# Kernel tuning notes

Measured on AMD Instinct MI355X. Metric: run time of the kernel, lower is better.

## Reference

```python
import jax, jax.numpy as jnp
import numpy as np

B, S, D = 2, 2048, 1024
H = 16
HD = D // H  # 64

def setup_inputs() -> dict:
    key = jax.random.key(0)
    ks = jax.random.split(key, 6)
    scale = 0.02
    x   = jax.random.normal(ks[0], (B, S, D), dtype=jnp.float32)
    Wq  = jax.random.normal(ks[1], (D, D), dtype=jnp.float32) * scale
    Wk  = jax.random.normal(ks[2], (D, D), dtype=jnp.float32) * scale
    Wv  = jax.random.normal(ks[3], (D, D), dtype=jnp.float32) * scale
    Wo  = jax.random.normal(ks[4], (D, D), dtype=jnp.float32) * scale
    bo  = jax.random.normal(ks[5], (D,), dtype=jnp.float32) * scale
    return {"x": x, "Wq": Wq, "Wk": Wk, "Wv": Wv, "Wo": Wo, "bo": bo}

def reference(x, Wq, Wk, Wv, Wo, bo):
    b, s, d = x.shape
    # QKV projections (no bias, qkv_bias=False); weights stored as [d_in, d_out]
    q = (x @ Wq).reshape(b, s, H, HD).transpose(0, 2, 1, 3)  # [b,h,s,hd]
    k = (x @ Wk).reshape(b, s, H, HD).transpose(0, 2, 1, 3)
    v = (x @ Wv).reshape(b, s, H, HD).transpose(0, 2, 1, 3)
    scores = jnp.einsum('bhqd,bhkd->bhqk', q, k)  # [b,h,s,s]
    causal = jnp.triu(jnp.ones((s, s), dtype=bool), k=1)
    scores = jnp.where(causal, -jnp.inf, scores)
    attn = jax.nn.softmax(scores / jnp.sqrt(jnp.float32(HD)), axis=-1)
    # dropout_rate = 0.0 -> identity
    ctx = jnp.einsum('bhqk,bhkd->bqhd', attn, v).reshape(b, s, d)
    return ctx @ Wo + bo
```

## Files before the change

kernel.cpp:

```cpp
#include <hip/hip_runtime.h>
#include <hip/hip_bf16.h>
#include <math.h>

#define B_ 2
#define S_ 2048
#define D_ 1024
#define H_ 16
#define HD_ 64
#define M_ (B_*S_)

typedef __attribute__((ext_vector_type(8))) short bf16x8;
typedef __attribute__((ext_vector_type(4))) float f32x4;

#define MFMA16(a,b,c) __builtin_amdgcn_mfma_f32_16x16x32_bf16(a,b,c,0,0,0)
#define INFF __builtin_inff()
#define LOG2E 1.44269504088896340736f
#define EXP2F(x) __builtin_amdgcn_exp2f(x)

static __device__ __forceinline__ unsigned short f2bf_bits(float f) {
    unsigned int u = __float_as_uint(f);
    unsigned int r = (u + 0x7fffu + ((u >> 16) & 1u)) >> 16;
    return (unsigned short)r;
}

static __device__ __forceinline__ unsigned cvt_pk_bf16(float a, float b) {
    unsigned r;
    asm("v_cvt_pk_bf16_f32 %0, %1, %2" : "=v"(r) : "v"(a), "v"(b));
    return r;
}

static __device__ __forceinline__ void gload16(const unsigned short* g, unsigned short* l) {
    __builtin_amdgcn_global_load_lds(
        (const __attribute__((address_space(1))) unsigned int*)(g),
        (__attribute__((address_space(3))) unsigned int*)(l),
        16, 0, 0);
}

#define BARR do { \
    __builtin_amdgcn_sched_barrier(0); \
    __builtin_amdgcn_s_barrier(); \
    __builtin_amdgcn_sched_barrier(0); \
} while (0)
#define LGK0 do { \
    asm volatile("s_waitcnt lgkmcnt(0)" ::: "memory"); \
    __builtin_amdgcn_sched_barrier(0); \
} while (0)
#define LGK8 do { \
    asm volatile("s_waitcnt lgkmcnt(8)" ::: "memory"); \
    __builtin_amdgcn_sched_barrier(0); \
} while (0)
#define VM6 do { \
    asm volatile("s_waitcnt vmcnt(6)" ::: "memory"); \
    __builtin_amdgcn_sched_barrier(0); \
} while (0)

__global__ __launch_bounds__(256) void convert_x_kernel(
    const float* __restrict__ x, unsigned short* __restrict__ o) {
    size_t i = (size_t)blockIdx.x * 256 + threadIdx.x;
    float4 v = reinterpret_cast<const float4*>(x)[i];
    ushort4 u;
    u.x = f2bf_bits(v.x); u.y = f2bf_bits(v.y);
    u.z = f2bf_bits(v.z); u.w = f2bf_bits(v.w);
    reinterpret_cast<ushort4*>(o)[i] = u;
}

__global__ __launch_bounds__(256) void convw_kernel(
    const float* __restrict__ W0, const float* __restrict__ W1,
    const float* __restrict__ W2, const float* __restrict__ W3,
    unsigned short* __restrict__ OT) {
    __shared__ float t[32][33];
    const float* W = (blockIdx.z == 0) ? W0 : (blockIdx.z == 1) ? W1
                    : (blockIdx.z == 2) ? W2 : W3;
    unsigned short* O = OT + (size_t)blockIdx.z * D_ * D_;
    int tx = threadIdx.x & 31, ty = threadIdx.x >> 5;
    int kb = blockIdx.y * 32, nb = blockIdx.x * 32;
#pragma unroll
    for (int i = 0; i < 4; i++)
        t[ty + 8*i][tx] = W[(size_t)(kb + ty + 8*i) * D_ + nb + tx];
    __syncthreads();
#pragma unroll
    for (int i = 0; i < 4; i++) {
        int n = nb + ty + 8*i, k = kb + tx;
        O[(size_t)n * D_ + k] = f2bf_bits(t[tx][ty + 8*i]);
    }
}

__global__ __launch_bounds__(512, 2) void gemm_qkv256(
    const unsigned short* __restrict__ A,
    const unsigned short* __restrict__ BT,
    unsigned short* __restrict__ outp)
{
    __shared__ union {
        struct { unsigned short A[2][2][8192]; unsigned short B[2][2][8192]; } s;
        unsigned short vt[256][136];
    } sm;
    const int tid = threadIdx.x, lane = tid & 63, wid = tid >> 6;
    const int lrow = lane & 15, lk8 = lane >> 4, orow = lk8 * 4;
    const int wmo = (wid >> 2) * 64;
    const int wno = (wid & 3) * 32;
    const int m0 = blockIdx.x * 256, n0 = blockIdx.y * 256;

    const int srow = lane >> 3, sgr = lane & 7;
    const unsigned sgo = (unsigned)(wid * 8 + srow) * 1024u
                       + (unsigned)((sgr ^ srow) << 3);
    const unsigned short* Ag = A  + (unsigned)m0 * 1024u + sgo;
    const unsigned short* Bg = BT + (unsigned)n0 * 1024u + sgo;
    const int ldsrb = wid * 512;

    const int sw0 = ((lk8 ^ (lrow & 7)) << 3);
    const int sw1 = (((4 | lk8) ^ (lrow & 7)) << 3);
    int ar[4], br[2];
#pragma unroll
    for (int f = 0; f < 4; f++) ar[f] = (wmo + f * 16 + lrow) * 64;
#pragma unroll
    for (int g = 0; g < 2; g++) br[g] = (wno + g * 16 + lrow) * 64;

    f32x4 acc[8][4] = {};
    bf16x8 af[4][2], bf0[2][2], bf1[2][2];

    auto stA = [&](int par, int mh, unsigned k) {
        unsigned short* d = &sm.s.A[par][mh][ldsrb];
        const unsigned short* g = Ag + (unsigned)mh * 131072u + k;
        gload16(g, d);
        gload16(g + 65536u, d + 4096);
    };
    auto stB = [&](int par, int nh, unsigned k) {
        unsigned short* d = &sm.s.B[par][nh][ldsrb];
        const unsigned short* g = Bg + (unsigned)nh * 131072u + k;
        gload16(g, d);
        gload16(g + 65536u, d + 4096);
    };
    auto lda = [&](int par, int mh) {
        const unsigned short* p = &sm.s.A[par][mh][0];
#pragma unroll
        for (int f = 0; f < 4; f++) {
            af[f][0] = *reinterpret_cast<const bf16x8*>(p + ar[f] + sw0);
            af[f][1] = *reinterpret_cast<const bf16x8*>(p + ar[f] + sw1);
        }
    };
    auto ldb0 = [&](int par, int nh) {
        const unsigned short* p = &sm.s.B[par][nh][0];
#pragma unroll
        for (int g = 0; g < 2; g++) {
            bf0[g][0] = *reinterpret_cast<const bf16x8*>(p + br[g] + sw0);
            bf0[g][1] = *reinterpret_cast<const bf16x8*>(p + br[g] + sw1);
        }
    };
    auto ldb1 = [&](int par, int nh) {
        const unsigned short* p = &sm.s.B[par][nh][0];
#pragma unroll
        for (int g = 0; g < 2; g++) {
            bf1[g][0] = *reinterpret_cast<const bf16x8*>(p + br[g] + sw0);
            bf1[g][1] = *reinterpret_cast<const bf16x8*>(p + br[g] + sw1);
        }
    };
    auto MMA0 = [&](int mh) {
        __builtin_amdgcn_s_setprio(1);
#pragma unroll
        for (int f = 0; f < 4; f++)
#pragma unroll
            for (int g = 0; g < 2; g++)
#pragma unroll
                for (int ks = 0; ks < 2; ks++)
                    acc[mh*4+f][g] = MFMA16(af[f][ks], bf0[g][ks], acc[mh*4+f][g]);
        __builtin_amdgcn_s_setprio(0);
    };
    auto MMA1 = [&](int mh) {
        __builtin_amdgcn_s_setprio(1);
#pragma unroll
        for (int f = 0; f < 4; f++)
#pragma unroll
            for (int g = 0; g < 2; g++)
#pragma unroll
                for (int ks = 0; ks < 2; ks++)
                    acc[mh*4+f][2+g] = MFMA16(af[f][ks], bf1[g][ks], acc[mh*4+f][2+g]);
        __builtin_amdgcn_s_setprio(0);
    };

    stA(0, 0, 0);  stB(0, 0, 0);  stB(0, 1, 0);  stA(0, 1, 0);
    stA(1, 0, 64); stB(1, 0, 64); stB(1, 1, 64);
    VM6; BARR;

#pragma unroll 1
    for (int i = 0; i < 8; i++) {
        const unsigned kA1 = (unsigned)(2*i + 1) * 64u;
        const unsigned k2  = (unsigned)((2*i + 2) & 15) * 64u;
        const unsigned k3  = (unsigned)((2*i + 3) & 15) * 64u;
        lda(0, 0); ldb0(0, 0); stA(1, 1, kA1);
        LGK8; BARR; LGK0; MMA0(0); BARR;
        ldb1(0, 1); stA(0, 0, k2);
        BARR; LGK0; MMA1(0); BARR;
        lda(0, 1); stB(0, 0, k2);
        BARR; LGK0; MMA1(1); BARR;
        stB(0, 1, k2);
        VM6; BARR; MMA0(1); BARR;
        lda(1, 0); ldb0(1, 0); stA(0, 1, k2);
        LGK8; BARR; LGK0; MMA0(0); BARR;
        ldb1(1, 1); stA(1, 0, k3);
        BARR; LGK0; MMA1(0); BARR;
        lda(1, 1); stB(1, 0, k3);
        BARR; LGK0; MMA1(1); BARR;
        stB(1, 1, k3);
        VM6; BARR; MMA0(1); BARR;
    }

    asm volatile("s_waitcnt vmcnt(0)" ::: "memory");
    __builtin_amdgcn_sched_barrier(0);
    __builtin_amdgcn_s_barrier();

    const int which = n0 >> 10;
    const int nl0 = n0 & 1023;
    const int bq = m0 >> 11;
    unsigned short* obase = outp + (size_t)which * 4194304;

    if (which < 2) {
        const float scale = (which == 0) ? (0.125f * LOG2E) : 1.0f;
#pragma unroll
        for (int fi = 0; fi < 8; fi++)
#pragma unroll
            for (int g = 0; g < 4; g++)
#pragma unroll
                for (int r = 0; r < 4; r++) {
                    int m = m0 + (fi >> 2) * 128 + wmo + (fi & 3) * 16 + orow + r;
                    int n = nl0 + (g >> 1) * 128 + wno + (g & 1) * 16 + lrow;
                    int s = m & 2047;
                    obase[(((size_t)(bq * 16 + (n >> 6)) * 2048 + s) << 6) + (n & 63)]
                        = f2bf_bits(acc[fi][g][r] * scale);
                }
    } else {
#pragma unroll
        for (int qm = 0; qm < 2; qm++) {
#pragma unroll
            for (int f = 0; f < 4; f++)
#pragma unroll
                for (int g = 0; g < 4; g++) {
                    const int ml = wmo + f * 16 + orow;
                    const int nc = (g >> 1) * 128 + wno + (g & 1) * 16 + lrow;
                    uint2 w;
                    w.x = cvt_pk_bf16(acc[qm*4+f][g][0], acc[qm*4+f][g][1]);
                    w.y = cvt_pk_bf16(acc[qm*4+f][g][2], acc[qm*4+f][g][3]);
                    *reinterpret_cast<uint2*>(&sm.vt[nc][ml]) = w;
                }
            __syncthreads();
            {
                const int row = tid >> 1, c0 = (tid & 1) * 64;
                unsigned short* dst = obase +
                    ((size_t)(bq * 1024) + nl0 + row) * 2048 +
                    (m0 & 2047) + qm * 128 + c0;
#pragma unroll
                for (int j = 0; j < 64; j += 8)
                    *reinterpret_cast<bf16x8*>(dst + j) =
                        *reinterpret_cast<const bf16x8*>(&sm.vt[row][c0 + j]);
            }
            __syncthreads();
        }
    }
}

template<int BN, int MODE>
__global__ __launch_bounds__(256) void gemm_gl(
    const unsigned short* __restrict__ A,
    const unsigned short* __restrict__ BT,
    void* __restrict__ outp,
    const float* __restrict__ bias)
{
    constexpr int K = 1024;
    constexpr int NF = (BN == 128) ? 4 : 2;
    __shared__ struct { unsigned short As[128][64]; unsigned short Bs[BN][64]; } sm;
    const int m0 = blockIdx.x * 128;
    const int n0 = blockIdx.y * BN;
    const int tid = threadIdx.x, lane = tid & 63, wid = tid >> 6;
    const int wm = (wid >> 1) * 64;
    const int wn = (wid & 1) * (BN / 2);
    const int lrow = lane & 15, lk8 = lane >> 4, orow = lk8 * 4;
    f32x4 acc[4][NF] = {};

    for (int k0 = 0; k0 < K; k0 += 64) {
#pragma unroll
        for (int i = 0; i < 4; i++) {
            const int rbase = wid * 32 + i * 8;
            const int rl = rbase + (lane >> 3);
            const int sc = ((lane & 7) ^ (rl & 7)) << 3;
            gload16(A + (size_t)(m0 + rl) * K + k0 + sc, &sm.As[rbase][0]);
        }
#pragma unroll
        for (int i = 0; i < BN / 32; i++) {
            const int rbase = wid * (BN / 4) + i * 8;
            const int rl = rbase + (lane >> 3);
            const int sc = ((lane & 7) ^ (rl & 7)) << 3;
            gload16(BT + (size_t)(n0 + rl) * K + k0 + sc, &sm.Bs[rbase][0]);
        }
        __syncthreads();
#pragma unroll
        for (int ks = 0; ks < 2; ks++) {
            bf16x8 af[4], bfr[NF];
#pragma unroll
            for (int f = 0; f < 4; f++) {
                const int row = wm + f * 16 + lrow;
                const int p = (ks * 4 + lk8) ^ (row & 7);
                af[f] = *reinterpret_cast<const bf16x8*>(&sm.As[row][p * 8]);
            }
#pragma unroll
            for (int f = 0; f < NF; f++) {
                const int row = wn + f * 16 + lrow;
                const int p = (ks * 4 + lk8) ^ (row & 7);
                bfr[f] = *reinterpret_cast<const bf16x8*>(&sm.Bs[row][p * 8]);
            }
            __builtin_amdgcn_s_setprio(1);
#pragma unroll
            for (int mf = 0; mf < 4; mf++)
#pragma unroll
                for (int nf = 0; nf < NF; nf++)
                    acc[mf][nf] = MFMA16(af[mf], bfr[nf], acc[mf][nf]);
            __builtin_amdgcn_s_setprio(0);
        }
        __syncthreads();
    }

    float* o = (float*)outp;
#pragma unroll
    for (int mf = 0; mf < 4; mf++)
#pragma unroll
        for (int nf = 0; nf < NF; nf++)
#pragma unroll
            for (int r = 0; r < 4; r++) {
                int m = m0 + wm + mf*16 + orow + r;
                int n = n0 + wn + nf*16 + lrow;
                o[(size_t)m * 1024 + n] = acc[mf][nf][r] + bias[n];
            }
}

__global__ __launch_bounds__(256, 4) void attn_kernel(
    const unsigned short* __restrict__ Q,
    const unsigned short* __restrict__ Kb,
    const unsigned short* __restrict__ VT,
    unsigned short* __restrict__ ctx)
{
    __shared__ unsigned short Ks[2][64][64];
    __shared__ unsigned short Vs[2][64][64];
    __shared__ unsigned short Pl[4][16][64];
    const int fid = blockIdx.x;
    const int xcd = fid & 7, t = fid >> 3;
    const int bh = xcd | ((t & 3) << 3);
    const int qt = 31 - (t >> 2);
    const int lane = threadIdx.x & 63, wid = threadIdx.x >> 6;
    const int lrow = lane & 15, lk8 = lane >> 4, orow = lk8 * 4;
    const unsigned short* Qp = Q  + (size_t)bh * (S_ * 64);
    const unsigned short* Kp = Kb + (size_t)bh * (S_ * 64);
    const unsigned short* Vp = VT + (size_t)bh * (64 * S_);
    const int b = bh >> 4, h = bh & 15;
    const int q0 = qt * 64 + wid * 16;
    const int nb = qt + 1;
    const int psw = (lrow & 7) << 3;

    auto stage = [&](int buf, int kv0) {
#pragma unroll
        for (int i = 0; i < 2; i++) {
            const int rbase = wid * 16 + 8 * i;
            const int rl = rbase + (lane >> 3);
            const int sc = (((lane & 7) ^ (rl & 7)) << 3);
            gload16(Kp + (size_t)(kv0 + rl) * 64 + sc, &Ks[buf][rbase][0]);
            gload16(Vp + (size_t)rl * S_ + kv0 + sc, &Vs[buf][rbase][0]);
        }
    };

    stage(0, 0);

    bf16x8 qf[2];
#pragma unroll
    for (int kt = 0; kt < 2; kt++)
        qf[kt] = *reinterpret_cast<const bf16x8*>(
            Qp + (size_t)(q0 + lrow) * 64 + kt*32 + lk8*8);

    f32x4 acc[4] = {};
    float lr = 0.f;

    __syncthreads();

#pragma unroll 1
    for (int kvb = 0; kvb < nb; kvb++) {
        const int cur = kvb & 1;
        if (kvb + 1 < nb) stage(cur ^ 1, (kvb + 1) * 64);

        f32x4 sacc[4] = {};
        __builtin_amdgcn_s_setprio(1);
#pragma unroll
        for (int kt = 0; kt < 2; kt++)
#pragma unroll
            for (int nf = 0; nf < 4; nf++) {
                const int row = nf * 16 + lrow;
                const int g = ((kt << 2) | lk8) ^ (row & 7);
                bf16x8 kf = *reinterpret_cast<const bf16x8*>(&Ks[cur][row][g << 3]);
                sacc[nf] = MFMA16(kf, qf[kt], sacc[nf]);
            }
        __builtin_amdgcn_s_setprio(0);
        if (kvb == qt) {
#pragma unroll
            for (int nf = 0; nf < 4; nf++)
#pragma unroll
                for (int r = 0; r < 4; r++)
                    if (nf*16 + orow + r > wid*16 + lrow) sacc[nf][r] = -INFF;
        }
        float ps[4];
#pragma unroll
        for (int nf = 0; nf < 4; nf++) {
#pragma unroll
            for (int r = 0; r < 4; r++)
                sacc[nf][r] = EXP2F(sacc[nf][r]);
            ps[nf] = (sacc[nf][0] + sacc[nf][1]) + (sacc[nf][2] + sacc[nf][3]);
        }
        lr += (ps[0] + ps[1]) + (ps[2] + ps[3]);
#pragma unroll
        for (int nf = 0; nf < 4; nf++) {
            uint2 w;
            w.x = cvt_pk_bf16(sacc[nf][0], sacc[nf][1]);
            w.y = cvt_pk_bf16(sacc[nf][2], sacc[nf][3]);
            *reinterpret_cast<uint2*>(&Pl[wid][lrow][(nf*16 + orow) ^ psw]) = w;
        }
        bf16x8 pf[2];
#pragma unroll
        for (int kt = 0; kt < 2; kt++)
            pf[kt] = *reinterpret_cast<const bf16x8*>(
                &Pl[wid][lrow][(kt*32 + lk8*8) ^ psw]);
        __builtin_amdgcn_s_setprio(1);
#pragma unroll
        for (int kt = 0; kt < 2; kt++)
#pragma unroll
            for (int nf = 0; nf < 4; nf++) {
                const int row = nf * 16 + lrow;
                const int g = ((kt << 2) | lk8) ^ (row & 7);
                bf16x8 vf = *reinterpret_cast<const bf16x8*>(&Vs[cur][row][g << 3]);
                acc[nf] = MFMA16(pf[kt], vf, acc[nf]);
            }
        __builtin_amdgcn_s_setprio(0);
        __syncthreads();
    }

    lr += __shfl_xor(lr, 16);
    lr += __shfl_xor(lr, 32);
    const float inv = 1.0f / lr;
#pragma unroll
    for (int r = 0; r < 4; r++) {
        const float linv = __shfl(inv, (lane & 48) + orow + r);
#pragma unroll
        for (int nf = 0; nf < 4; nf++) {
            int s = q0 + orow + r;
            int col = h * 64 + nf * 16 + lrow;
            ctx[((size_t)(b * S_ + s)) * D_ + col] = f2bf_bits(acc[nf][r] * linv);
        }
    }
}

extern "C" void kernel_launch(void* const* d_in, const int* in_sizes, int n_in,
                              void* d_out, int out_size, void* d_ws, size_t ws_size,
                              hipStream_t stream) {
    const float* x  = (const float*)d_in[0];
    const float* Wq = (const float*)d_in[1];
    const float* Wk = (const float*)d_in[2];
    const float* Wv = (const float*)d_in[3];
    const float* Wo = (const float*)d_in[4];
    const float* bo = (const float*)d_in[5];
    float* out = (float*)d_out;

    char* ws = (char*)d_ws;
    unsigned short* xb  = (unsigned short*)(ws);
    unsigned short* WT  = (unsigned short*)(ws + 8388608);
    unsigned short* QKV = (unsigned short*)(ws + 16777216);
    unsigned short* ctx = (unsigned short*)(ws + 41943040);

    unsigned short* Qb  = QKV;
    unsigned short* Kb  = QKV + 4194304;
    unsigned short* VTb = QKV + 8388608;

    convert_x_kernel<<<dim3(4096), dim3(256), 0, stream>>>(x, xb);
    convw_kernel<<<dim3(32, 32, 4), dim3(256), 0, stream>>>(Wq, Wk, Wv, Wo, WT);

    gemm_qkv256<<<dim3(16, 12), dim3(512), 0, stream>>>(xb, WT, QKV);

    attn_kernel<<<dim3(1024), dim3(256), 0, stream>>>(Qb, Kb, VTb, ctx);

    gemm_gl<64, 1><<<dim3(32, 16), dim3(256), 0, stream>>>(
        ctx, WT + 3145728, (void*)out, bo);
}
```

Before: 99.48 us.

## Use 32x32 MFMA with 128-row query tiles and register-resident P in attention

Attention now uses 32x32x16 bf16 MFMAs, with each wave owning 32 query rows and each block owning 128 queries, which halves the grid. The P matrix stays in registers: v_permlane32_swap rearranges it instead of a round trip through LDS, removing the Pl buffer and its LDS traffic. Each K/V tile staged into LDS is reused across twice as many queries. The output projection GEMM switches to a 128-wide tile with half the grid. Fewer blocks and lower occupancy (launch bounds 2) may reduce latency hiding and worsen load balance on the causal triangle.

```diff
diff --git a/kernel.cpp b/kernel.cpp
--- a/kernel.cpp
+++ b/kernel.cpp
@@ -11,8 +11,10 @@
 
 typedef __attribute__((ext_vector_type(8))) short bf16x8;
 typedef __attribute__((ext_vector_type(4))) float f32x4;
+typedef __attribute__((ext_vector_type(16))) float f32x16;
 
 #define MFMA16(a,b,c) __builtin_amdgcn_mfma_f32_16x16x32_bf16(a,b,c,0,0,0)
+#define MFMA32(a,b,c) __builtin_amdgcn_mfma_f32_32x32x16_bf16(a,b,c,0,0,0)
 #define INFF __builtin_inff()
 #define LOG2E 1.44269504088896340736f
 #define EXP2F(x) __builtin_amdgcn_exp2f(x)
@@ -330,7 +332,7 @@
             }
 }
 
-__global__ __launch_bounds__(256, 4) void attn_kernel(
+__global__ __launch_bounds__(256, 2) void attn_kernel(
     const unsigned short* __restrict__ Q,
     const unsigned short* __restrict__ Kb,
     const unsigned short* __restrict__ VT,
@@ -338,20 +340,19 @@
 {
     __shared__ unsigned short Ks[2][64][64];
     __shared__ unsigned short Vs[2][64][64];
-    __shared__ unsigned short Pl[4][16][64];
     const int fid = blockIdx.x;
     const int xcd = fid & 7, t = fid >> 3;
     const int bh = xcd | ((t & 3) << 3);
-    const int qt = 31 - (t >> 2);
+    const int qt = 15 - (t >> 2);
     const int lane = threadIdx.x & 63, wid = threadIdx.x >> 6;
-    const int lrow = lane & 15, lk8 = lane >> 4, orow = lk8 * 4;
+    const int l31 = lane & 31, hi = lane >> 5;
     const unsigned short* Qp = Q  + (size_t)bh * (S_ * 64);
     const unsigned short* Kp = Kb + (size_t)bh * (S_ * 64);
     const unsigned short* Vp = VT + (size_t)bh * (64 * S_);
     const int b = bh >> 4, h = bh & 15;
-    const int q0 = qt * 64 + wid * 16;
-    const int nb = qt + 1;
-    const int psw = (lrow & 7) << 3;
+    const int q0w = qt * 128 + wid * 32;
+    const int qg  = q0w + l31;
+    const int nb  = 2 * qt + 2;
 
     auto stage = [&](int buf, int kv0) {
 #pragma unroll
@@ -366,14 +367,16 @@
 
     stage(0, 0);
 
-    bf16x8 qf[2];
-#pragma unroll
-    for (int kt = 0; kt < 2; kt++)
-        qf[kt] = *reinterpret_cast<const bf16x8*>(
-            Qp + (size_t)(q0 + lrow) * 64 + kt*32 + lk8*8);
-
-    f32x4 acc[4] = {};
+    bf16x8 qf[4];
+#pragma unroll
+    for (int c = 0; c < 4; c++)
+        qf[c] = *reinterpret_cast<const bf16x8*>(
+            Qp + (size_t)qg * 64 + c * 16 + hi * 8);
+
+    f32x16 oacc0 = {}, oacc1 = {};
     float lr = 0.f;
+    const int r0 = l31, r1 = 32 + l31;
+    const int g0 = r0 & 7, g1 = r1 & 7;
 
     __syncthreads();
 
@@ -382,73 +385,88 @@
         const int cur = kvb & 1;
         if (kvb + 1 < nb) stage(cur ^ 1, (kvb + 1) * 64);
 
-        f32x4 sacc[4] = {};
+        f32x16 s0 = {}, s1 = {};
         __builtin_amdgcn_s_setprio(1);
 #pragma unroll
-        for (int kt = 0; kt < 2; kt++)
-#pragma unroll
-            for (int nf = 0; nf < 4; nf++) {
-                const int row = nf * 16 + lrow;
-                const int g = ((kt << 2) | lk8) ^ (row & 7);
-                bf16x8 kf = *reinterpret_cast<const bf16x8*>(&Ks[cur][row][g << 3]);
-                sacc[nf] = MFMA16(kf, qf[kt], sacc[nf]);
+        for (int c = 0; c < 4; c++) {
+            const int gg = (c << 1) | hi;
+            bf16x8 k0 = *reinterpret_cast<const bf16x8*>(&Ks[cur][r0][(gg ^ g0) << 3]);
+            bf16x8 k1 = *reinterpret_cast<const bf16x8*>(&Ks[cur][r1][(gg ^ g1) << 3]);
+            s0 = MFMA32(k0, qf[c], s0);
+            s1 = MFMA32(k1, qf[c], s1);
+        }
+        __builtin_amdgcn_s_setprio(0);
+
+        if (kvb * 64 + 63 > q0w) {
+            const int kvb64 = kvb * 64 + 4 * hi;
+#pragma unroll
+            for (int reg = 0; reg < 16; reg++) {
+                const int kv = kvb64 + (reg & 3) + 8 * (reg >> 2);
+                if (kv > qg)      s0[reg] = -INFF;
+                if (kv + 32 > qg) s1[reg] = -INFF;
             }
-        __builtin_amdgcn_s_setprio(0);
-        if (kvb == qt) {
-#pragma unroll
-            for (int nf = 0; nf < 4; nf++)
-#pragma unroll
-                for (int r = 0; r < 4; r++)
-                    if (nf*16 + orow + r > wid*16 + lrow) sacc[nf][r] = -INFF;
-        }
-        float ps[4];
-#pragma unroll
-        for (int nf = 0; nf < 4; nf++) {
-#pragma unroll
-            for (int r = 0; r < 4; r++)
-                sacc[nf][r] = EXP2F(sacc[nf][r]);
-            ps[nf] = (sacc[nf][0] + sacc[nf][1]) + (sacc[nf][2] + sacc[nf][3]);
-        }
-        lr += (ps[0] + ps[1]) + (ps[2] + ps[3]);
-#pragma unroll
-        for (int nf = 0; nf < 4; nf++) {
-            uint2 w;
-            w.x = cvt_pk_bf16(sacc[nf][0], sacc[nf][1]);
-            w.y = cvt_pk_bf16(sacc[nf][2], sacc[nf][3]);
-            *reinterpret_cast<uint2*>(&Pl[wid][lrow][(nf*16 + orow) ^ psw]) = w;
-        }
-        bf16x8 pf[2];
-#pragma unroll
-        for (int kt = 0; kt < 2; kt++)
-            pf[kt] = *reinterpret_cast<const bf16x8*>(
-                &Pl[wid][lrow][(kt*32 + lk8*8) ^ psw]);
+        }
+
+        float t0 = 0.f, t1 = 0.f;
+#pragma unroll
+        for (int reg = 0; reg < 16; reg++) {
+            s0[reg] = EXP2F(s0[reg]);
+            s1[reg] = EXP2F(s1[reg]);
+            t0 += s0[reg];
+            t1 += s1[reg];
+        }
+        lr += t0 + t1;
+
+        bf16x8 pf[4];
+#pragma unroll
+        for (int c = 0; c < 4; c++) {
+            const int rb = (c & 1) * 8;
+            unsigned x0, x1, y0, y1;
+            if (c < 2) {
+                x0 = cvt_pk_bf16(s0[rb+0], s0[rb+1]);
+                x1 = cvt_pk_bf16(s0[rb+2], s0[rb+3]);
+                y0 = cvt_pk_bf16(s0[rb+4], s0[rb+5]);
+                y1 = cvt_pk_bf16(s0[rb+6], s0[rb+7]);
+            } else {
+                x0 = cvt_pk_bf16(s1[rb+0], s1[rb+1]);
+                x1 = cvt_pk_bf16(s1[rb+2], s1[rb+3]);
+                y0 = cvt_pk_bf16(s1[rb+4], s1[rb+5]);
+                y1 = cvt_pk_bf16(s1[rb+6], s1[rb+7]);
+            }
+            asm("v_permlane32_swap_b32 %0, %1" : "+v"(x0), "+v"(y0));
+            asm("v_permlane32_swap_b32 %0, %1" : "+v"(x1), "+v"(y1));
+            union { unsigned u[4]; bf16x8 v; } pk;
+            pk.u[0] = x0; pk.u[1] = x1; pk.u[2] = y0; pk.u[3] = y1;
+            pf[c] = pk.v;
+        }
+
         __builtin_amdgcn_s_setprio(1);
 #pragma unroll
-        for (int kt = 0; kt < 2; kt++)
-#pragma unroll
-            for (int nf = 0; nf < 4; nf++) {
-                const int row = nf * 16 + lrow;
-                const int g = ((kt << 2) | lk8) ^ (row & 7);
-                bf16x8 vf = *reinterpret_cast<const bf16x8*>(&Vs[cur][row][g << 3]);
-                acc[nf] = MFMA16(pf[kt], vf, acc[nf]);
-            }
+        for (int c = 0; c < 4; c++) {
+            const int gg = (c << 1) | hi;
+            bf16x8 v0 = *reinterpret_cast<const bf16x8*>(&Vs[cur][r0][(gg ^ g0) << 3]);
+            bf16x8 v1 = *reinterpret_cast<const bf16x8*>(&Vs[cur][r1][(gg ^ g1) << 3]);
+            oacc0 = MFMA32(v0, pf[c], oacc0);
+            oacc1 = MFMA32(v1, pf[c], oacc1);
+        }
         __builtin_amdgcn_s_setprio(0);
         __syncthreads();
     }
 
-    lr += __shfl_xor(lr, 16);
     lr += __shfl_xor(lr, 32);
     const float inv = 1.0f / lr;
-#pragma unroll
-    for (int r = 0; r < 4; r++) {
-        const float linv = __shfl(inv, (lane & 48) + orow + r);
-#pragma unroll
-        for (int nf = 0; nf < 4; nf++) {
-            int s = q0 + orow + r;
-            int col = h * 64 + nf * 16 + lrow;
-            ctx[((size_t)(b * S_ + s)) * D_ + col] = f2bf_bits(acc[nf][r] * linv);
-        }
-    }
+    unsigned short* crow = ctx + ((size_t)(b * S_ + qg)) * D_ + h * 64;
+#pragma unroll
+    for (int a = 0; a < 4; a++)
+#pragma unroll
+        for (int p = 0; p < 2; p++) {
+            const int reg = 4 * a + 2 * p;
+            const int col = 8 * a + 4 * hi + 2 * p;
+            unsigned w0 = cvt_pk_bf16(oacc0[reg] * inv, oacc0[reg + 1] * inv);
+            unsigned w1 = cvt_pk_bf16(oacc1[reg] * inv, oacc1[reg + 1] * inv);
+            *reinterpret_cast<unsigned*>(crow + col)      = w0;
+            *reinterpret_cast<unsigned*>(crow + 32 + col) = w1;
+        }
 }
 
 extern "C" void kernel_launch(void* const* d_in, const int* in_sizes, int n_in,
@@ -477,8 +495,8 @@
 
     gemm_qkv256<<<dim3(16, 12), dim3(512), 0, stream>>>(xb, WT, QKV);
 
-    attn_kernel<<<dim3(1024), dim3(256), 0, stream>>>(Qb, Kb, VTb, ctx);
-
-    gemm_gl<64, 1><<<dim3(32, 16), dim3(256), 0, stream>>>(
+    attn_kernel<<<dim3(512), dim3(256), 0, stream>>>(Qb, Kb, VTb, ctx);
+
+    gemm_gl<128, 1><<<dim3(32, 8), dim3(256), 0, stream>>>(
         ctx, WT + 3145728, (void*)out, bo);
 }
```

Measured after the change: 111.8 us. 12.4% more time.
